# Optimization experiments

Measured on AMD Instinct MI355X. Metric: run time of the kernel, lower is better.

## Reference

```python
import jax, jax.numpy as jnp
import numpy as np

NUM_SPIXELS = 256
N_ITER = 3
TEMP = 1.0


def setup_inputs() -> dict:
    key = jax.random.key(0)
    features = jax.random.normal(key, (4, 16, 256, 256), dtype=jnp.float32)
    return {"features": features}


def reference(features):
    B, C, H, W = features.shape
    dt = features.dtype
    # torch.linspace(0, h-1, h)/h == arange(h)/h
    y = jnp.arange(H, dtype=dt) / H
    x = jnp.arange(W, dtype=dt) / W
    mesh_y, mesh_x = jnp.meshgrid(y, x, indexing='ij')  # each [H, W]
    xy = jnp.stack([mesh_x, mesh_y], axis=0)            # [2, H, W]
    xy_b = jnp.broadcast_to(xy, (B, 2, H, W))

    pixel = jnp.concatenate([features, xy_b], axis=1).reshape(B, C + 2, H * W)
    p = pixel.transpose(0, 2, 1)  # [B, N, D], D = C+2

    s = max(1, int(NUM_SPIXELS ** 0.5))
    # adaptive_avg_pool2d to (s, s); H, W divisible by s -> exact block mean
    def pool(t):
        D = t.shape[1]
        return t.reshape(B, D, s, H // s, s, W // s).mean(axis=(3, 5)).reshape(B, D, s * s)

    centers = jnp.concatenate([pool(features), pool(xy_b)], axis=1)  # [B, D, M]
    c = centers.transpose(0, 2, 1)  # [B, M, D]

    Q = None
    for i in range(N_ITER):
        # Euclidean cdist: ||p||^2 + ||c||^2 - 2 p.c, clipped and sqrt'ed
        d2 = (jnp.sum(p * p, axis=-1)[:, :, None]
              + jnp.sum(c * c, axis=-1)[:, None, :]
              - 2.0 * jnp.einsum('bnd,bmd->bnm', p, c))
        dist = jnp.sqrt(jnp.maximum(d2, 1e-12))  # [B, N, M]
        Q = jax.nn.softmax(-dist * TEMP, axis=-1)
        if i < N_ITER - 1:
            norm = jnp.sum(Q, axis=1)[:, :, None] + 1e-6        # [B, M, 1]
            c = jnp.einsum('bnm,bnd->bmd', Q, p) / norm         # [B, M, D]

    centers_feat = c[:, :, :C].transpose(0, 2, 1)  # [B, C, M]
    return Q, centers_feat
```

## Files before the change

kernel.cpp:

```cpp
#include <hip/hip_runtime.h>
#include <math.h>

#define BB 4
#define CC 16
#define HH 256
#define WW 256
#define NN (HH*WW)
#define MM 256
#define CROW 20
#define PROW 20
#define PIX 32
#define TSUB 4
#define PIXPERBLK (PIX*TSUB)
#define CHUNKS (NN/PIXPERBLK)

typedef float f32x2 __attribute__((ext_vector_type(2)));

__device__ __forceinline__ f32x2 mk2(float a, float b) { f32x2 r; r.x = a; r.y = b; return r; }
__device__ __forceinline__ f32x2 pk_fma(f32x2 a, f32x2 b, f32x2 c) {
    return __builtin_elementwise_fma(a, b, c);
}

__global__ void init_centers(const float* __restrict__ feat, float* __restrict__ cbuf)
{
    const int b    = blockIdx.x >> 8;
    const int m    = blockIdx.x & 255;
    const int lane = threadIdx.x;
    const int sy = m >> 4, sx = m & 15;

    float cvals[16];
#pragma unroll
    for (int d = 0; d < 16; ++d) {
        float v = 0.f;
#pragma unroll
        for (int k = 0; k < 4; ++k) {
            int q  = lane + (k << 6);
            int py = q >> 4, px = q & 15;
            int n  = (sy*16 + py)*WW + sx*16 + px;
            v += feat[((b*CC + d) << 16) + n];
        }
#pragma unroll
        for (int off = 32; off; off >>= 1) v += __shfl_down(v, off);
        cvals[d] = v * (1.f/256.f);
    }
    if (lane == 0) {
        float* row = cbuf + (b*MM + m)*CROW;
        float cn2 = 0.f;
#pragma unroll
        for (int d = 0; d < 16; ++d) { row[d] = cvals[d]; cn2 = fmaf(cvals[d], cvals[d], cn2); }
        float cx = (sx*16 + 7.5f) * (1.f/256.f);
        float cy = (sy*16 + 7.5f) * (1.f/256.f);
        row[16] = cx; row[17] = cy;
        cn2 = fmaf(cx, cx, cn2);
        cn2 = fmaf(cy, cy, cn2);
        row[18] = cn2;
        row[19] = 0.f;
    }
}

__global__ void build_pt(const float* __restrict__ feat, float* __restrict__ ptbuf)
{
    const int b = blockIdx.x >> 8;
    const int n = ((blockIdx.x & 255) << 8) | threadIdx.x;
    float v[16];
#pragma unroll
    for (int d = 0; d < 16; ++d) v[d] = feat[((b*CC + d) << 16) + n];
    float x = (float)(n & 255) * (1.f/256.f);
    float y = (float)(n >> 8) * (1.f/256.f);
    float pn2 = 0.f;
#pragma unroll
    for (int d = 0; d < 16; ++d) pn2 = fmaf(v[d], v[d], pn2);
    pn2 = fmaf(x, x, pn2);
    pn2 = fmaf(y, y, pn2);
    float4* row = reinterpret_cast<float4*>(ptbuf + (size_t)(b*NN + n)*PROW);
    row[0] = make_float4(v[0],  v[1],  v[2],  v[3]);
    row[1] = make_float4(v[4],  v[5],  v[6],  v[7]);
    row[2] = make_float4(v[8],  v[9],  v[10], v[11]);
    row[3] = make_float4(v[12], v[13], v[14], v[15]);
    row[4] = make_float4(x, y, pn2, 1.0f);
}

template<bool FINAL>
__global__ __launch_bounds__(256, 3)
void ssn_iter(const float* __restrict__ ptbuf, const float* __restrict__ cbuf,
              float* __restrict__ wout)
{
    __shared__ __align__(16) float pls[PIXPERBLK*PROW];
    __shared__ float ssum_s[TSUB][4][16];
    __shared__ float w_s[TSUB][PIX];
    __shared__ float xfer[FINAL ? 4 : 128*41];

    const int tid    = threadIdx.x;
    const int b      = blockIdx.x >> 9;
    const int chunk  = blockIdx.x & (CHUNKS-1);
    const int n_base = chunk * PIXPERBLK;
    const int lane   = tid & 63;
    const int wv     = tid >> 6;
    const int mlo    = tid & 127;
    const int pxbase = (tid >> 7) << 4;

    {
        const float4* src = reinterpret_cast<const float4*>(
            ptbuf + (size_t)(b*NN + n_base)*PROW);
#pragma unroll
        for (int k = 0; k < 3; ++k) {
            int f = tid + (k << 8);
            if (f < PIXPERBLK*PROW/4)
                reinterpret_cast<float4*>(pls)[f] = src[f];
        }
    }

    f32x2 cp0[9], cp1[9]; float cn20, cn21;
    {
        const float4* cv = reinterpret_cast<const float4*>(cbuf + (b*MM + mlo)*CROW);
        float4 a0 = cv[0], a1 = cv[1], a2 = cv[2], a3 = cv[3], a4 = cv[4];
        cp0[0]=mk2(a0.x,a0.y); cp0[1]=mk2(a0.z,a0.w);
        cp0[2]=mk2(a1.x,a1.y); cp0[3]=mk2(a1.z,a1.w);
        cp0[4]=mk2(a2.x,a2.y); cp0[5]=mk2(a2.z,a2.w);
        cp0[6]=mk2(a3.x,a3.y); cp0[7]=mk2(a3.z,a3.w);
        cp0[8]=mk2(a4.x,a4.y); cn20=a4.z;
    }
    {
        const float4* cv = reinterpret_cast<const float4*>(cbuf + (b*MM + mlo + 128)*CROW);
        float4 a0 = cv[0], a1 = cv[1], a2 = cv[2], a3 = cv[3], a4 = cv[4];
        cp1[0]=mk2(a0.x,a0.y); cp1[1]=mk2(a0.z,a0.w);
        cp1[2]=mk2(a1.x,a1.y); cp1[3]=mk2(a1.z,a1.w);
        cp1[4]=mk2(a2.x,a2.y); cp1[5]=mk2(a2.z,a2.w);
        cp1[6]=mk2(a3.x,a3.y); cp1[7]=mk2(a3.z,a3.w);
        cp1[8]=mk2(a4.x,a4.y); cn21=a4.z;
    }

    f32x2 acc0[10], acc1[10];
    if (!FINAL) {
#pragma unroll
        for (int k = 0; k < 10; ++k) { acc0[k] = mk2(0.f,0.f); acc1[k] = mk2(0.f,0.f); }
    }

    const int pxo4 = ((lane&1)<<3) | ((lane&2)<<1) | ((lane&4)>>1) | ((lane&8)>>3);

    __syncthreads();

    for (int t = 0; t < TSUB; ++t) {
        float e0[16], e1[16];
#pragma unroll
        for (int k = 0; k < 16; ++k) {
            const float4* pv = reinterpret_cast<const float4*>(
                &pls[(t*PIX + pxbase + k)*PROW]);
            float4 q0 = pv[0], q1 = pv[1], q2 = pv[2], q3 = pv[3], q4 = pv[4];
            f32x2 u0=mk2(q0.x,q0.y), u1=mk2(q0.z,q0.w), u2=mk2(q1.x,q1.y),
                  u3=mk2(q1.z,q1.w), u4=mk2(q2.x,q2.y), u5=mk2(q2.z,q2.w),
                  u6=mk2(q3.x,q3.y), u7=mk2(q3.z,q3.w), u8=mk2(q4.x,q4.y);
            f32x2 d0 = mk2(0.f,0.f), d1 = mk2(0.f,0.f);
            d0 = pk_fma(u0, cp0[0], d0);  d1 = pk_fma(u0, cp1[0], d1);
            d0 = pk_fma(u1, cp0[1], d0);  d1 = pk_fma(u1, cp1[1], d1);
            d0 = pk_fma(u2, cp0[2], d0);  d1 = pk_fma(u2, cp1[2], d1);
            d0 = pk_fma(u3, cp0[3], d0);  d1 = pk_fma(u3, cp1[3], d1);
            d0 = pk_fma(u4, cp0[4], d0);  d1 = pk_fma(u4, cp1[4], d1);
            d0 = pk_fma(u5, cp0[5], d0);  d1 = pk_fma(u5, cp1[5], d1);
            d0 = pk_fma(u6, cp0[6], d0);  d1 = pk_fma(u6, cp1[6], d1);
            d0 = pk_fma(u7, cp0[7], d0);  d1 = pk_fma(u7, cp1[7], d1);
            d0 = pk_fma(u8, cp0[8], d0);  d1 = pk_fma(u8, cp1[8], d1);
            float d20 = fmaf(-2.f, d0.x + d0.y, q4.z + cn20);
            float d21 = fmaf(-2.f, d1.x + d1.y, q4.z + cn21);
            e0[k] = __expf(-__builtin_amdgcn_sqrtf(fmaxf(d20, 1e-12f)));
            e1[k] = __expf(-__builtin_amdgcn_sqrtf(fmaxf(d21, 1e-12f)));
        }

        float s[8];
        {
            const bool hi = (lane & 1);
#pragma unroll
            for (int k = 0; k < 8; ++k) {
                float a  = e0[k]   + e1[k];
                float bq = e0[k+8] + e1[k+8];
                float recv = __shfl_xor(hi ? a : bq, 1);
                s[k] = (hi ? bq : a) + recv;
            }
        }
#define RS_ROUND(MASK, H) { const bool hi = (lane & (MASK)); \
        _Pragma("unroll") \
        for (int k = 0; k < (H); ++k) { \
            float a = s[k], bq = s[k+(H)]; \
            float recv = __shfl_xor(hi ? a : bq, (MASK)); \
            s[k] = (hi ? bq : a) + recv; } }
        RS_ROUND(2, 4)
        RS_ROUND(4, 2)
        RS_ROUND(8, 1)
#undef RS_ROUND
        s[0] += __shfl_xor(s[0], 16);
        s[0] += __shfl_xor(s[0], 32);
        if (lane < 16) ssum_s[t][wv][pxo4] = s[0];
        __syncthreads();
        if (tid < 32) {
            int h = tid >> 4, p4 = tid & 15;
            w_s[t][tid] = 1.0f / (ssum_s[t][2*h][p4] + ssum_s[t][2*h+1][p4]);
        }
        __syncthreads();

        if (FINAL) {
#pragma unroll
            for (int k = 0; k < 16; ++k) {
                float w = w_s[t][pxbase + k];
                size_t rowoff = ((size_t)(b*NN + n_base + t*PIX + pxbase + k) << 8);
                wout[rowoff + mlo]       = e0[k] * w;
                wout[rowoff + mlo + 128] = e1[k] * w;
            }
        } else {
#pragma unroll
            for (int k = 0; k < 16; ++k) {
                const float4* pv = reinterpret_cast<const float4*>(
                    &pls[(t*PIX + pxbase + k)*PROW]);
                float4 q0 = pv[0], q1 = pv[1], q2 = pv[2], q3 = pv[3], q4 = pv[4];
                float w = w_s[t][pxbase + k];
                float w0 = e0[k]*w, w1 = e1[k]*w;
                f32x2 ew0 = mk2(w0, w0), ew1 = mk2(w1, w1);
                f32x2 u0=mk2(q0.x,q0.y), u1=mk2(q0.z,q0.w), u2=mk2(q1.x,q1.y),
                      u3=mk2(q1.z,q1.w), u4=mk2(q2.x,q2.y), u5=mk2(q2.z,q2.w),
                      u6=mk2(q3.x,q3.y), u7=mk2(q3.z,q3.w), u8=mk2(q4.x,q4.y),
                      u9=mk2(q4.z,q4.w);
                acc0[0] = pk_fma(ew0, u0, acc0[0]);  acc1[0] = pk_fma(ew1, u0, acc1[0]);
                acc0[1] = pk_fma(ew0, u1, acc0[1]);  acc1[1] = pk_fma(ew1, u1, acc1[1]);
                acc0[2] = pk_fma(ew0, u2, acc0[2]);  acc1[2] = pk_fma(ew1, u2, acc1[2]);
                acc0[3] = pk_fma(ew0, u3, acc0[3]);  acc1[3] = pk_fma(ew1, u3, acc1[3]);
                acc0[4] = pk_fma(ew0, u4, acc0[4]);  acc1[4] = pk_fma(ew1, u4, acc1[4]);
                acc0[5] = pk_fma(ew0, u5, acc0[5]);  acc1[5] = pk_fma(ew1, u5, acc1[5]);
                acc0[6] = pk_fma(ew0, u6, acc0[6]);  acc1[6] = pk_fma(ew1, u6, acc1[6]);
                acc0[7] = pk_fma(ew0, u7, acc0[7]);  acc1[7] = pk_fma(ew1, u7, acc1[7]);
                acc0[8] = pk_fma(ew0, u8, acc0[8]);  acc1[8] = pk_fma(ew1, u8, acc1[8]);
                acc0[9] = pk_fma(ew0, u9, acc0[9]);  acc1[9] = pk_fma(ew1, u9, acc1[9]);
            }
        }
    }

    if (!FINAL) {
        if (tid >= 128) {
            float* xb = &xfer[(tid - 128)*41];
#pragma unroll
            for (int j = 0; j < 10; ++j) { xb[2*j]    = acc0[j].x; xb[2*j+1]    = acc0[j].y; }
#pragma unroll
            for (int j = 0; j < 10; ++j) { xb[20+2*j] = acc1[j].x; xb[20+2*j+1] = acc1[j].y; }
        }
        __syncthreads();
        if (tid < 128) {
            const float* xb = &xfer[tid*41];
#pragma unroll
            for (int j = 0; j < 10; ++j) { acc0[j].x += xb[2*j];    acc0[j].y += xb[2*j+1]; }
#pragma unroll
            for (int j = 0; j < 10; ++j) { acc1[j].x += xb[20+2*j]; acc1[j].y += xb[20+2*j+1]; }

            float* dst0 = wout + ((size_t)(b*CHUNKS + chunk)*MM + mlo)*PROW;
            float4* v0 = reinterpret_cast<float4*>(dst0);
            v0[0] = make_float4(acc0[0].x, acc0[0].y, acc0[1].x, acc0[1].y);
            v0[1] = make_float4(acc0[2].x, acc0[2].y, acc0[3].x, acc0[3].y);
            v0[2] = make_float4(acc0[4].x, acc0[4].y, acc0[5].x, acc0[5].y);
            v0[3] = make_float4(acc0[6].x, acc0[6].y, acc0[7].x, acc0[7].y);
            v0[4] = make_float4(acc0[8].x, acc0[8].y, acc0[9].y, 0.f);

            float* dst1 = wout + ((size_t)(b*CHUNKS + chunk)*MM + mlo + 128)*PROW;
            float4* v1 = reinterpret_cast<float4*>(dst1);
            v1[0] = make_float4(acc1[0].x, acc1[0].y, acc1[1].x, acc1[1].y);
            v1[1] = make_float4(acc1[2].x, acc1[2].y, acc1[3].x, acc1[3].y);
            v1[2] = make_float4(acc1[4].x, acc1[4].y, acc1[5].x, acc1[5].y);
            v1[3] = make_float4(acc1[6].x, acc1[6].y, acc1[7].x, acc1[7].y);
            v1[4] = make_float4(acc1[8].x, acc1[8].y, acc1[9].y, 0.f);
        }
    }
}

__global__ __launch_bounds__(256)
void reduce_finalize(const float* __restrict__ pp, float* __restrict__ cbuf,
                     float* __restrict__ cfout, int write_cf)
{
    const int b   = blockIdx.x >> 8;
    const int m   = blockIdx.x & 255;
    const int tid = threadIdx.x;
    const int lane = tid & 63, wv = tid >> 6;

    const float4* r0 = reinterpret_cast<const float4*>(
        pp + ((size_t)(b*CHUNKS + tid)*MM + m)*PROW);
    const float4* r1 = reinterpret_cast<const float4*>(
        pp + ((size_t)(b*CHUNKS + tid + 256)*MM + m)*PROW);
    float a[19];
    {
        float4 u0=r0[0], u1=r0[1], u2=r0[2], u3=r0[3], u4=r0[4];
        float4 w0=r1[0], w1=r1[1], w2=r1[2], w3=r1[3], w4=r1[4];
        a[0]=u0.x+w0.x;  a[1]=u0.y+w0.y;  a[2]=u0.z+w0.z;  a[3]=u0.w+w0.w;
        a[4]=u1.x+w1.x;  a[5]=u1.y+w1.y;  a[6]=u1.z+w1.z;  a[7]=u1.w+w1.w;
        a[8]=u2.x+w2.x;  a[9]=u2.y+w2.y;  a[10]=u2.z+w2.z; a[11]=u2.w+w2.w;
        a[12]=u3.x+w3.x; a[13]=u3.y+w3.y; a[14]=u3.z+w3.z; a[15]=u3.w+w3.w;
        a[16]=u4.x+w4.x; a[17]=u4.y+w4.y; a[18]=u4.z+w4.z;
    }
#pragma unroll
    for (int off = 32; off; off >>= 1) {
#pragma unroll
        for (int d = 0; d < 19; ++d) a[d] += __shfl_down(a[d], off);
    }

    __shared__ float red[4][20];
    if (lane == 0) {
#pragma unroll
        for (int d = 0; d < 19; ++d) red[wv][d] = a[d];
    }
    __syncthreads();
    if (tid == 0) {
        float s[19];
#pragma unroll
        for (int d = 0; d < 19; ++d)
            s[d] = red[0][d] + red[1][d] + red[2][d] + red[3][d];
        float den = s[18] + 1e-6f;
        float* row = cbuf + (b*MM + m)*CROW;
        float cn2 = 0.f;
#pragma unroll
        for (int d = 0; d < 18; ++d) {
            float cv = s[d] / den;
            row[d] = cv;
            cn2 = fmaf(cv, cv, cn2);
            if (write_cf && d < 16) cfout[((b*CC + d) << 8) + m] = cv;
        }
        row[18] = cn2;
        row[19] = 0.f;
    }
}

extern "C" void kernel_launch(void* const* d_in, const int* in_sizes, int n_in,
                              void* d_out, int out_size, void* d_ws, size_t ws_size,
                              hipStream_t stream)
{
    const float* feat = (const float*)d_in[0];
    float* dout = (float*)d_out;

    float* cbuf  = (float*)d_ws;
    float* ptbuf = cbuf + 32768;
    float* pp    = ptbuf + (size_t)BB*NN*PROW;

    float* qout  = dout;
    float* cfout = dout + (size_t)BB*NN*MM;

    build_pt<<<dim3(BB*256), dim3(256), 0, stream>>>(feat, ptbuf);
    init_centers<<<dim3(BB*MM), dim3(64), 0, stream>>>(feat, cbuf);

    for (int it = 0; it < 2; ++it) {
        ssn_iter<false><<<dim3(BB*CHUNKS), dim3(256), 0, stream>>>(ptbuf, cbuf, pp);
        reduce_finalize<<<dim3(BB*MM), dim3(256), 0, stream>>>(pp, cbuf, cfout, it == 1);
    }
    ssn_iter<true><<<dim3(BB*CHUNKS), dim3(256), 0, stream>>>(ptbuf, cbuf, qout);
}
```

Measured before the change: 273.7 us.

## Split final SSN pass into dedicated kernel with 4-centers-per-thread mapping

Splits the templated iteration kernel in two: an unchanged non-final kernel and a new final kernel that writes the soft-assignment matrix Q. In the final kernel each thread handles 4 centers strided by 16 and 8 pixels strided by 4, replacing the old 2 centers by 16 contiguous pixels. The shuffle reduction and shared-memory row-sum layout are reworked to match. The aim is to change the Q store pattern and the per-thread work split in the write-bound final pass, at the cost of more center registers per thread and a new reduction mapping.

```diff
diff --git a/kernel.cpp b/kernel.cpp
--- a/kernel.cpp
+++ b/kernel.cpp
@@ -80,15 +80,14 @@
     row[4] = make_float4(x, y, pn2, 1.0f);
 }
 
-template<bool FINAL>
 __global__ __launch_bounds__(256, 3)
-void ssn_iter(const float* __restrict__ ptbuf, const float* __restrict__ cbuf,
-              float* __restrict__ wout)
+void ssn_nf(const float* __restrict__ ptbuf, const float* __restrict__ cbuf,
+            float* __restrict__ pp)
 {
     __shared__ __align__(16) float pls[PIXPERBLK*PROW];
     __shared__ float ssum_s[TSUB][4][16];
     __shared__ float w_s[TSUB][PIX];
-    __shared__ float xfer[FINAL ? 4 : 128*41];
+    __shared__ float xfer[128*41];
 
     const int tid    = threadIdx.x;
     const int b      = blockIdx.x >> 9;
@@ -131,10 +130,8 @@
     }
 
     f32x2 acc0[10], acc1[10];
-    if (!FINAL) {
-#pragma unroll
-        for (int k = 0; k < 10; ++k) { acc0[k] = mk2(0.f,0.f); acc1[k] = mk2(0.f,0.f); }
-    }
+#pragma unroll
+    for (int k = 0; k < 10; ++k) { acc0[k] = mk2(0.f,0.f); acc1[k] = mk2(0.f,0.f); }
 
     const int pxo4 = ((lane&1)<<3) | ((lane&2)<<1) | ((lane&4)>>1) | ((lane&8)>>3);
 
@@ -197,72 +194,180 @@
         }
         __syncthreads();
 
-        if (FINAL) {
-#pragma unroll
-            for (int k = 0; k < 16; ++k) {
-                float w = w_s[t][pxbase + k];
-                size_t rowoff = ((size_t)(b*NN + n_base + t*PIX + pxbase + k) << 8);
-                wout[rowoff + mlo]       = e0[k] * w;
-                wout[rowoff + mlo + 128] = e1[k] * w;
-            }
-        } else {
-#pragma unroll
-            for (int k = 0; k < 16; ++k) {
-                const float4* pv = reinterpret_cast<const float4*>(
-                    &pls[(t*PIX + pxbase + k)*PROW]);
-                float4 q0 = pv[0], q1 = pv[1], q2 = pv[2], q3 = pv[3], q4 = pv[4];
-                float w = w_s[t][pxbase + k];
-                float w0 = e0[k]*w, w1 = e1[k]*w;
-                f32x2 ew0 = mk2(w0, w0), ew1 = mk2(w1, w1);
-                f32x2 u0=mk2(q0.x,q0.y), u1=mk2(q0.z,q0.w), u2=mk2(q1.x,q1.y),
-                      u3=mk2(q1.z,q1.w), u4=mk2(q2.x,q2.y), u5=mk2(q2.z,q2.w),
-                      u6=mk2(q3.x,q3.y), u7=mk2(q3.z,q3.w), u8=mk2(q4.x,q4.y),
-                      u9=mk2(q4.z,q4.w);
-                acc0[0] = pk_fma(ew0, u0, acc0[0]);  acc1[0] = pk_fma(ew1, u0, acc1[0]);
-                acc0[1] = pk_fma(ew0, u1, acc0[1]);  acc1[1] = pk_fma(ew1, u1, acc1[1]);
-                acc0[2] = pk_fma(ew0, u2, acc0[2]);  acc1[2] = pk_fma(ew1, u2, acc1[2]);
-                acc0[3] = pk_fma(ew0, u3, acc0[3]);  acc1[3] = pk_fma(ew1, u3, acc1[3]);
-                acc0[4] = pk_fma(ew0, u4, acc0[4]);  acc1[4] = pk_fma(ew1, u4, acc1[4]);
-                acc0[5] = pk_fma(ew0, u5, acc0[5]);  acc1[5] = pk_fma(ew1, u5, acc1[5]);
-                acc0[6] = pk_fma(ew0, u6, acc0[6]);  acc1[6] = pk_fma(ew1, u6, acc1[6]);
-                acc0[7] = pk_fma(ew0, u7, acc0[7]);  acc1[7] = pk_fma(ew1, u7, acc1[7]);
-                acc0[8] = pk_fma(ew0, u8, acc0[8]);  acc1[8] = pk_fma(ew1, u8, acc1[8]);
-                acc0[9] = pk_fma(ew0, u9, acc0[9]);  acc1[9] = pk_fma(ew1, u9, acc1[9]);
-            }
-        }
-    }
-
-    if (!FINAL) {
-        if (tid >= 128) {
-            float* xb = &xfer[(tid - 128)*41];
-#pragma unroll
-            for (int j = 0; j < 10; ++j) { xb[2*j]    = acc0[j].x; xb[2*j+1]    = acc0[j].y; }
-#pragma unroll
-            for (int j = 0; j < 10; ++j) { xb[20+2*j] = acc1[j].x; xb[20+2*j+1] = acc1[j].y; }
+#pragma unroll
+        for (int k = 0; k < 16; ++k) {
+            const float4* pv = reinterpret_cast<const float4*>(
+                &pls[(t*PIX + pxbase + k)*PROW]);
+            float4 q0 = pv[0], q1 = pv[1], q2 = pv[2], q3 = pv[3], q4 = pv[4];
+            float w = w_s[t][pxbase + k];
+            float w0 = e0[k]*w, w1 = e1[k]*w;
+            f32x2 ew0 = mk2(w0, w0), ew1 = mk2(w1, w1);
+            f32x2 u0=mk2(q0.x,q0.y), u1=mk2(q0.z,q0.w), u2=mk2(q1.x,q1.y),
+                  u3=mk2(q1.z,q1.w), u4=mk2(q2.x,q2.y), u5=mk2(q2.z,q2.w),
+                  u6=mk2(q3.x,q3.y), u7=mk2(q3.z,q3.w), u8=mk2(q4.x,q4.y),
+                  u9=mk2(q4.z,q4.w);
+            acc0[0] = pk_fma(ew0, u0, acc0[0]);  acc1[0] = pk_fma(ew1, u0, acc1[0]);
+            acc0[1] = pk_fma(ew0, u1, acc0[1]);  acc1[1] = pk_fma(ew1, u1, acc1[1]);
+            acc0[2] = pk_fma(ew0, u2, acc0[2]);  acc1[2] = pk_fma(ew1, u2, acc1[2]);
+            acc0[3] = pk_fma(ew0, u3, acc0[3]);  acc1[3] = pk_fma(ew1, u3, acc1[3]);
+            acc0[4] = pk_fma(ew0, u4, acc0[4]);  acc1[4] = pk_fma(ew1, u4, acc1[4]);
+            acc0[5] = pk_fma(ew0, u5, acc0[5]);  acc1[5] = pk_fma(ew1, u5, acc1[5]);
+            acc0[6] = pk_fma(ew0, u6, acc0[6]);  acc1[6] = pk_fma(ew1, u6, acc1[6]);
+            acc0[7] = pk_fma(ew0, u7, acc0[7]);  acc1[7] = pk_fma(ew1, u7, acc1[7]);
+            acc0[8] = pk_fma(ew0, u8, acc0[8]);  acc1[8] = pk_fma(ew1, u8, acc1[8]);
+            acc0[9] = pk_fma(ew0, u9, acc0[9]);  acc1[9] = pk_fma(ew1, u9, acc1[9]);
+        }
+    }
+
+    if (tid >= 128) {
+        float* xb = &xfer[(tid - 128)*41];
+#pragma unroll
+        for (int j = 0; j < 10; ++j) { xb[2*j]    = acc0[j].x; xb[2*j+1]    = acc0[j].y; }
+#pragma unroll
+        for (int j = 0; j < 10; ++j) { xb[20+2*j] = acc1[j].x; xb[20+2*j+1] = acc1[j].y; }
+    }
+    __syncthreads();
+    if (tid < 128) {
+        const float* xb = &xfer[tid*41];
+#pragma unroll
+        for (int j = 0; j < 10; ++j) { acc0[j].x += xb[2*j];    acc0[j].y += xb[2*j+1]; }
+#pragma unroll
+        for (int j = 0; j < 10; ++j) { acc1[j].x += xb[20+2*j]; acc1[j].y += xb[20+2*j+1]; }
+
+        float* dst0 = pp + ((size_t)(b*CHUNKS + chunk)*MM + mlo)*PROW;
+        float4* v0 = reinterpret_cast<float4*>(dst0);
+        v0[0] = make_float4(acc0[0].x, acc0[0].y, acc0[1].x, acc0[1].y);
+        v0[1] = make_float4(acc0[2].x, acc0[2].y, acc0[3].x, acc0[3].y);
+        v0[2] = make_float4(acc0[4].x, acc0[4].y, acc0[5].x, acc0[5].y);
+        v0[3] = make_float4(acc0[6].x, acc0[6].y, acc0[7].x, acc0[7].y);
+        v0[4] = make_float4(acc0[8].x, acc0[8].y, acc0[9].y, 0.f);
+
+        float* dst1 = pp + ((size_t)(b*CHUNKS + chunk)*MM + mlo + 128)*PROW;
+        float4* v1 = reinterpret_cast<float4*>(dst1);
+        v1[0] = make_float4(acc1[0].x, acc1[0].y, acc1[1].x, acc1[1].y);
+        v1[1] = make_float4(acc1[2].x, acc1[2].y, acc1[3].x, acc1[3].y);
+        v1[2] = make_float4(acc1[4].x, acc1[4].y, acc1[5].x, acc1[5].y);
+        v1[3] = make_float4(acc1[6].x, acc1[6].y, acc1[7].x, acc1[7].y);
+        v1[4] = make_float4(acc1[8].x, acc1[8].y, acc1[9].y, 0.f);
+    }
+}
+
+__global__ __launch_bounds__(256, 3)
+void ssn_fin(const float* __restrict__ ptbuf, const float* __restrict__ cbuf,
+             float* __restrict__ qout)
+{
+    __shared__ __align__(16) float pls[PIXPERBLK*PROW];
+    __shared__ float ssum_s[TSUB][4][PIX];
+    __shared__ float w_s[TSUB][PIX];
+
+    const int tid    = threadIdx.x;
+    const int b      = blockIdx.x >> 9;
+    const int chunk  = blockIdx.x & (CHUNKS-1);
+    const int n_base = chunk * PIXPERBLK;
+    const int L      = tid & 63;
+    const int wv     = tid >> 6;
+    const int g      = L & 3;
+    const int msub   = L >> 2;
+    const int mbase  = wv*64 + msub;
+
+    {
+        const float4* src = reinterpret_cast<const float4*>(
+            ptbuf + (size_t)(b*NN + n_base)*PROW);
+#pragma unroll
+        for (int k = 0; k < 3; ++k) {
+            int f = tid + (k << 8);
+            if (f < PIXPERBLK*PROW/4)
+                reinterpret_cast<float4*>(pls)[f] = src[f];
+        }
+    }
+
+    f32x2 cp[4][9]; float cn2[4];
+#pragma unroll
+    for (int j = 0; j < 4; ++j) {
+        const float4* cv = reinterpret_cast<const float4*>(
+            cbuf + (b*MM + mbase + 16*j)*CROW);
+        float4 a0 = cv[0], a1 = cv[1], a2 = cv[2], a3 = cv[3], a4 = cv[4];
+        cp[j][0]=mk2(a0.x,a0.y); cp[j][1]=mk2(a0.z,a0.w);
+        cp[j][2]=mk2(a1.x,a1.y); cp[j][3]=mk2(a1.z,a1.w);
+        cp[j][4]=mk2(a2.x,a2.y); cp[j][5]=mk2(a2.z,a2.w);
+        cp[j][6]=mk2(a3.x,a3.y); cp[j][7]=mk2(a3.z,a3.w);
+        cp[j][8]=mk2(a4.x,a4.y); cn2[j]=a4.z;
+    }
+
+    __syncthreads();
+
+    for (int t = 0; t < TSUB; ++t) {
+        float e[4][8];
+#pragma unroll
+        for (int k = 0; k < 8; ++k) {
+            const int row = t*PIX + g + 4*k;
+            const float4* pv = reinterpret_cast<const float4*>(&pls[row*PROW]);
+            float4 q0 = pv[0], q1 = pv[1], q2 = pv[2], q3 = pv[3], q4 = pv[4];
+            f32x2 u0=mk2(q0.x,q0.y), u1=mk2(q0.z,q0.w), u2=mk2(q1.x,q1.y),
+                  u3=mk2(q1.z,q1.w), u4=mk2(q2.x,q2.y), u5=mk2(q2.z,q2.w),
+                  u6=mk2(q3.x,q3.y), u7=mk2(q3.z,q3.w), u8=mk2(q4.x,q4.y);
+            f32x2 d0=mk2(0.f,0.f), d1=mk2(0.f,0.f), d2v=mk2(0.f,0.f), d3=mk2(0.f,0.f);
+            d0 = pk_fma(u0, cp[0][0], d0); d1 = pk_fma(u0, cp[1][0], d1);
+            d2v= pk_fma(u0, cp[2][0], d2v);d3 = pk_fma(u0, cp[3][0], d3);
+            d0 = pk_fma(u1, cp[0][1], d0); d1 = pk_fma(u1, cp[1][1], d1);
+            d2v= pk_fma(u1, cp[2][1], d2v);d3 = pk_fma(u1, cp[3][1], d3);
+            d0 = pk_fma(u2, cp[0][2], d0); d1 = pk_fma(u2, cp[1][2], d1);
+            d2v= pk_fma(u2, cp[2][2], d2v);d3 = pk_fma(u2, cp[3][2], d3);
+            d0 = pk_fma(u3, cp[0][3], d0); d1 = pk_fma(u3, cp[1][3], d1);
+            d2v= pk_fma(u3, cp[2][3], d2v);d3 = pk_fma(u3, cp[3][3], d3);
+            d0 = pk_fma(u4, cp[0][4], d0); d1 = pk_fma(u4, cp[1][4], d1);
+            d2v= pk_fma(u4, cp[2][4], d2v);d3 = pk_fma(u4, cp[3][4], d3);
+            d0 = pk_fma(u5, cp[0][5], d0); d1 = pk_fma(u5, cp[1][5], d1);
+            d2v= pk_fma(u5, cp[2][5], d2v);d3 = pk_fma(u5, cp[3][5], d3);
+            d0 = pk_fma(u6, cp[0][6], d0); d1 = pk_fma(u6, cp[1][6], d1);
+            d2v= pk_fma(u6, cp[2][6], d2v);d3 = pk_fma(u6, cp[3][6], d3);
+            d0 = pk_fma(u7, cp[0][7], d0); d1 = pk_fma(u7, cp[1][7], d1);
+            d2v= pk_fma(u7, cp[2][7], d2v);d3 = pk_fma(u7, cp[3][7], d3);
+            d0 = pk_fma(u8, cp[0][8], d0); d1 = pk_fma(u8, cp[1][8], d1);
+            d2v= pk_fma(u8, cp[2][8], d2v);d3 = pk_fma(u8, cp[3][8], d3);
+            float s0 = fmaf(-2.f, d0.x + d0.y, q4.z + cn2[0]);
+            float s1 = fmaf(-2.f, d1.x + d1.y, q4.z + cn2[1]);
+            float s2 = fmaf(-2.f, d2v.x + d2v.y, q4.z + cn2[2]);
+            float s3 = fmaf(-2.f, d3.x + d3.y, q4.z + cn2[3]);
+            e[0][k] = __expf(-__builtin_amdgcn_sqrtf(fmaxf(s0, 1e-12f)));
+            e[1][k] = __expf(-__builtin_amdgcn_sqrtf(fmaxf(s1, 1e-12f)));
+            e[2][k] = __expf(-__builtin_amdgcn_sqrtf(fmaxf(s2, 1e-12f)));
+            e[3][k] = __expf(-__builtin_amdgcn_sqrtf(fmaxf(s3, 1e-12f)));
+        }
+
+        float s[8];
+#pragma unroll
+        for (int k = 0; k < 8; ++k)
+            s[k] = (e[0][k] + e[1][k]) + (e[2][k] + e[3][k]);
+#define RS_ROUND(MASK, H) { const bool hi = (L & (MASK)); \
+        _Pragma("unroll") \
+        for (int k = 0; k < (H); ++k) { \
+            float a = s[k], bq = s[k+(H)]; \
+            float recv = __shfl_xor(hi ? a : bq, (MASK)); \
+            s[k] = (hi ? bq : a) + recv; } }
+        RS_ROUND(4, 4)
+        RS_ROUND(8, 2)
+        RS_ROUND(16, 1)
+#undef RS_ROUND
+        s[0] += __shfl_xor(s[0], 32);
+        {
+            const int kown = (((L>>2)&1)<<2) | (((L>>3)&1)<<1) | ((L>>4)&1);
+            if (L < 32) ssum_s[t][wv][g + 4*kown] = s[0];
         }
         __syncthreads();
-        if (tid < 128) {
-            const float* xb = &xfer[tid*41];
-#pragma unroll
-            for (int j = 0; j < 10; ++j) { acc0[j].x += xb[2*j];    acc0[j].y += xb[2*j+1]; }
-#pragma unroll
-            for (int j = 0; j < 10; ++j) { acc1[j].x += xb[20+2*j]; acc1[j].y += xb[20+2*j+1]; }
-
-            float* dst0 = wout + ((size_t)(b*CHUNKS + chunk)*MM + mlo)*PROW;
-            float4* v0 = reinterpret_cast<float4*>(dst0);
-            v0[0] = make_float4(acc0[0].x, acc0[0].y, acc0[1].x, acc0[1].y);
-            v0[1] = make_float4(acc0[2].x, acc0[2].y, acc0[3].x, acc0[3].y);
-            v0[2] = make_float4(acc0[4].x, acc0[4].y, acc0[5].x, acc0[5].y);
-            v0[3] = make_float4(acc0[6].x, acc0[6].y, acc0[7].x, acc0[7].y);
-            v0[4] = make_float4(acc0[8].x, acc0[8].y, acc0[9].y, 0.f);
-
-            float* dst1 = wout + ((size_t)(b*CHUNKS + chunk)*MM + mlo + 128)*PROW;
-            float4* v1 = reinterpret_cast<float4*>(dst1);
-            v1[0] = make_float4(acc1[0].x, acc1[0].y, acc1[1].x, acc1[1].y);
-            v1[1] = make_float4(acc1[2].x, acc1[2].y, acc1[3].x, acc1[3].y);
-            v1[2] = make_float4(acc1[4].x, acc1[4].y, acc1[5].x, acc1[5].y);
-            v1[3] = make_float4(acc1[6].x, acc1[6].y, acc1[7].x, acc1[7].y);
-            v1[4] = make_float4(acc1[8].x, acc1[8].y, acc1[9].y, 0.f);
+        if (tid < 32) {
+            w_s[t][tid] = 1.0f / (ssum_s[t][0][tid] + ssum_s[t][1][tid]
+                                + ssum_s[t][2][tid] + ssum_s[t][3][tid]);
+        }
+        __syncthreads();
+
+#pragma unroll
+        for (int k = 0; k < 8; ++k) {
+            float w = w_s[t][g + 4*k];
+            size_t rowoff = ((size_t)(b*NN + n_base + t*PIX + g + 4*k)) << 8;
+#pragma unroll
+            for (int j = 0; j < 4; ++j)
+                qout[rowoff + mbase + 16*j] = e[j][k] * w;
         }
     }
 }
@@ -340,8 +445,8 @@
     init_centers<<<dim3(BB*MM), dim3(64), 0, stream>>>(feat, cbuf);
 
     for (int it = 0; it < 2; ++it) {
-        ssn_iter<false><<<dim3(BB*CHUNKS), dim3(256), 0, stream>>>(ptbuf, cbuf, pp);
+        ssn_nf<<<dim3(BB*CHUNKS), dim3(256), 0, stream>>>(ptbuf, cbuf, pp);
         reduce_finalize<<<dim3(BB*MM), dim3(256), 0, stream>>>(pp, cbuf, cfout, it == 1);
     }
-    ssn_iter<true><<<dim3(BB*CHUNKS), dim3(256), 0, stream>>>(ptbuf, cbuf, qout);
-}
+    ssn_fin<<<dim3(BB*CHUNKS), dim3(256), 0, stream>>>(ptbuf, cbuf, qout);
+}
```

Result: no change. 275.1 us (+0.5%).

## Compute final-iteration distances with split-bf16 MFMA in a dedicated kernel

Applied to the files above, without the earlier changes.

Splits the templated iteration kernel into a non-final kernel (unchanged logic) and a new final kernel. The final kernel computes pixel-center dot products with 16x16x32 bf16 MFMA, using a hi/lo bf16 split (three MFMAs) to approximate fp32 accuracy. It then does the exp/softmax normalization and writes Q. This moves the dot-product work from packed FMA to matrix cores, at the cost of some precision and per-pixel conversion overhead.

```diff
diff --git a/kernel.cpp b/kernel.cpp
--- a/kernel.cpp
+++ b/kernel.cpp
@@ -15,10 +15,22 @@
 #define CHUNKS (NN/PIXPERBLK)
 
 typedef float f32x2 __attribute__((ext_vector_type(2)));
+typedef float f32x4v __attribute__((ext_vector_type(4)));
+typedef short bf16x8 __attribute__((ext_vector_type(8)));
 
 __device__ __forceinline__ f32x2 mk2(float a, float b) { f32x2 r; r.x = a; r.y = b; return r; }
 __device__ __forceinline__ f32x2 pk_fma(f32x2 a, f32x2 b, f32x2 c) {
     return __builtin_elementwise_fma(a, b, c);
+}
+
+__device__ __forceinline__ unsigned short f2bf(float f) {
+    unsigned u = __builtin_bit_cast(unsigned, f);
+    unsigned r = (u + 0x7FFFu + ((u >> 16) & 1u)) >> 16;
+    return (unsigned short)r;
+}
+__device__ __forceinline__ float bf2f(unsigned short v) {
+    unsigned u = ((unsigned)v) << 16;
+    return __builtin_bit_cast(float, u);
 }
 
 __global__ void init_centers(const float* __restrict__ feat, float* __restrict__ cbuf)
@@ -80,15 +92,14 @@
     row[4] = make_float4(x, y, pn2, 1.0f);
 }
 
-template<bool FINAL>
 __global__ __launch_bounds__(256, 3)
-void ssn_iter(const float* __restrict__ ptbuf, const float* __restrict__ cbuf,
-              float* __restrict__ wout)
+void ssn_nf(const float* __restrict__ ptbuf, const float* __restrict__ cbuf,
+            float* __restrict__ pp)
 {
     __shared__ __align__(16) float pls[PIXPERBLK*PROW];
     __shared__ float ssum_s[TSUB][4][16];
     __shared__ float w_s[TSUB][PIX];
-    __shared__ float xfer[FINAL ? 4 : 128*41];
+    __shared__ float xfer[128*41];
 
     const int tid    = threadIdx.x;
     const int b      = blockIdx.x >> 9;
@@ -131,10 +142,8 @@
     }
 
     f32x2 acc0[10], acc1[10];
-    if (!FINAL) {
-#pragma unroll
-        for (int k = 0; k < 10; ++k) { acc0[k] = mk2(0.f,0.f); acc1[k] = mk2(0.f,0.f); }
-    }
+#pragma unroll
+    for (int k = 0; k < 10; ++k) { acc0[k] = mk2(0.f,0.f); acc1[k] = mk2(0.f,0.f); }
 
     const int pxo4 = ((lane&1)<<3) | ((lane&2)<<1) | ((lane&4)>>1) | ((lane&8)>>3);
 
@@ -197,72 +206,203 @@
         }
         __syncthreads();
 
-        if (FINAL) {
-#pragma unroll
-            for (int k = 0; k < 16; ++k) {
-                float w = w_s[t][pxbase + k];
-                size_t rowoff = ((size_t)(b*NN + n_base + t*PIX + pxbase + k) << 8);
-                wout[rowoff + mlo]       = e0[k] * w;
-                wout[rowoff + mlo + 128] = e1[k] * w;
+#pragma unroll
+        for (int k = 0; k < 16; ++k) {
+            const float4* pv = reinterpret_cast<const float4*>(
+                &pls[(t*PIX + pxbase + k)*PROW]);
+            float4 q0 = pv[0], q1 = pv[1], q2 = pv[2], q3 = pv[3], q4 = pv[4];
+            float w = w_s[t][pxbase + k];
+            float w0 = e0[k]*w, w1 = e1[k]*w;
+            f32x2 ew0 = mk2(w0, w0), ew1 = mk2(w1, w1);
+            f32x2 u0=mk2(q0.x,q0.y), u1=mk2(q0.z,q0.w), u2=mk2(q1.x,q1.y),
+                  u3=mk2(q1.z,q1.w), u4=mk2(q2.x,q2.y), u5=mk2(q2.z,q2.w),
+                  u6=mk2(q3.x,q3.y), u7=mk2(q3.z,q3.w), u8=mk2(q4.x,q4.y),
+                  u9=mk2(q4.z,q4.w);
+            acc0[0] = pk_fma(ew0, u0, acc0[0]);  acc1[0] = pk_fma(ew1, u0, acc1[0]);
+            acc0[1] = pk_fma(ew0, u1, acc0[1]);  acc1[1] = pk_fma(ew1, u1, acc1[1]);
+            acc0[2] = pk_fma(ew0, u2, acc0[2]);  acc1[2] = pk_fma(ew1, u2, acc1[2]);
+            acc0[3] = pk_fma(ew0, u3, acc0[3]);  acc1[3] = pk_fma(ew1, u3, acc1[3]);
+            acc0[4] = pk_fma(ew0, u4, acc0[4]);  acc1[4] = pk_fma(ew1, u4, acc1[4]);
+            acc0[5] = pk_fma(ew0, u5, acc0[5]);  acc1[5] = pk_fma(ew1, u5, acc1[5]);
+            acc0[6] = pk_fma(ew0, u6, acc0[6]);  acc1[6] = pk_fma(ew1, u6, acc1[6]);
+            acc0[7] = pk_fma(ew0, u7, acc0[7]);  acc1[7] = pk_fma(ew1, u7, acc1[7]);
+            acc0[8] = pk_fma(ew0, u8, acc0[8]);  acc1[8] = pk_fma(ew1, u8, acc1[8]);
+            acc0[9] = pk_fma(ew0, u9, acc0[9]);  acc1[9] = pk_fma(ew1, u9, acc1[9]);
+        }
+    }
+
+    if (tid >= 128) {
+        float* xb = &xfer[(tid - 128)*41];
+#pragma unroll
+        for (int j = 0; j < 10; ++j) { xb[2*j]    = acc0[j].x; xb[2*j+1]    = acc0[j].y; }
+#pragma unroll
+        for (int j = 0; j < 10; ++j) { xb[20+2*j] = acc1[j].x; xb[20+2*j+1] = acc1[j].y; }
+    }
+    __syncthreads();
+    if (tid < 128) {
+        const float* xb = &xfer[tid*41];
+#pragma unroll
+        for (int j = 0; j < 10; ++j) { acc0[j].x += xb[2*j];    acc0[j].y += xb[2*j+1]; }
+#pragma unroll
+        for (int j = 0; j < 10; ++j) { acc1[j].x += xb[20+2*j]; acc1[j].y += xb[20+2*j+1]; }
+
+        float* dst0 = pp + ((size_t)(b*CHUNKS + chunk)*MM + mlo)*PROW;
+        float4* v0 = reinterpret_cast<float4*>(dst0);
+        v0[0] = make_float4(acc0[0].x, acc0[0].y, acc0[1].x, acc0[1].y);
+        v0[1] = make_float4(acc0[2].x, acc0[2].y, acc0[3].x, acc0[3].y);
+        v0[2] = make_float4(acc0[4].x, acc0[4].y, acc0[5].x, acc0[5].y);
+        v0[3] = make_float4(acc0[6].x, acc0[6].y, acc0[7].x, acc0[7].y);
+        v0[4] = make_float4(acc0[8].x, acc0[8].y, acc0[9].y, 0.f);
+
+        float* dst1 = pp + ((size_t)(b*CHUNKS + chunk)*MM + mlo + 128)*PROW;
+        float4* v1 = reinterpret_cast<float4*>(dst1);
+        v1[0] = make_float4(acc1[0].x, acc1[0].y, acc1[1].x, acc1[1].y);
+        v1[1] = make_float4(acc1[2].x, acc1[2].y, acc1[3].x, acc1[3].y);
+        v1[2] = make_float4(acc1[4].x, acc1[4].y, acc1[5].x, acc1[5].y);
+        v1[3] = make_float4(acc1[6].x, acc1[6].y, acc1[7].x, acc1[7].y);
+        v1[4] = make_float4(acc1[8].x, acc1[8].y, acc1[9].y, 0.f);
+    }
+}
+
+__global__ __launch_bounds__(256, 3)
+void ssn_fin(const float* __restrict__ ptbuf, const float* __restrict__ cbuf,
+             float* __restrict__ qout)
+{
+    __shared__ __align__(16) float pls[PIXPERBLK*PROW];
+    __shared__ float ssum_s[4][32];
+    __shared__ float w_s[32];
+
+    const int tid    = threadIdx.x;
+    const int b      = blockIdx.x >> 9;
+    const int chunk  = blockIdx.x & (CHUNKS-1);
+    const int n_base = chunk * PIXPERBLK;
+    const int L      = tid & 63;
+    const int wv     = tid >> 6;
+    const int g      = L >> 4;
+    const int al     = L & 15;
+
+    {
+        const float4* src = reinterpret_cast<const float4*>(
+            ptbuf + (size_t)(b*NN + n_base)*PROW);
+#pragma unroll
+        for (int k = 0; k < 3; ++k) {
+            int f = tid + (k << 8);
+            if (f < PIXPERBLK*PROW/4)
+                reinterpret_cast<float4*>(pls)[f] = src[f];
+        }
+    }
+
+    bf16x8 bhi[4], blo[4]; float cn2m[4];
+#pragma unroll
+    for (int mt = 0; mt < 4; ++mt) {
+        const float* crow = cbuf + (size_t)(b*MM + wv*64 + mt*16 + al)*CROW;
+        float bf_[8];
+#pragma unroll
+        for (int j = 0; j < 8; ++j) bf_[j] = 0.f;
+        if (g < 2) {
+            float4 c0 = *reinterpret_cast<const float4*>(crow + 8*g);
+            float4 c1 = *reinterpret_cast<const float4*>(crow + 8*g + 4);
+            bf_[0]=c0.x; bf_[1]=c0.y; bf_[2]=c0.z; bf_[3]=c0.w;
+            bf_[4]=c1.x; bf_[5]=c1.y; bf_[6]=c1.z; bf_[7]=c1.w;
+        } else if (g == 2) {
+            float4 c0 = *reinterpret_cast<const float4*>(crow + 16);
+            bf_[0]=c0.x; bf_[1]=c0.y;
+        }
+#pragma unroll
+        for (int j = 0; j < 8; ++j) {
+            unsigned short h = f2bf(bf_[j]);
+            bhi[mt][j] = (short)h;
+            blo[mt][j] = (short)f2bf(bf_[j] - bf2f(h));
+        }
+        cn2m[mt] = crow[18];
+    }
+
+    __syncthreads();
+
+#pragma unroll
+    for (int pair = 0; pair < 4; ++pair) {
+        float e[2][4][4];
+        float part[2][4];
+
+#pragma unroll
+        for (int h = 0; h < 2; ++h) {
+            const int pxt = pair*32 + h*16;
+
+            float af[8];
+#pragma unroll
+            for (int j = 0; j < 8; ++j) af[j] = 0.f;
+            const int abase = (pxt + al)*PROW;
+            if (g < 2) {
+                float4 x0 = *reinterpret_cast<const float4*>(&pls[abase + 8*g]);
+                float4 x1 = *reinterpret_cast<const float4*>(&pls[abase + 8*g + 4]);
+                af[0]=x0.x; af[1]=x0.y; af[2]=x0.z; af[3]=x0.w;
+                af[4]=x1.x; af[5]=x1.y; af[6]=x1.z; af[7]=x1.w;
+            } else if (g == 2) {
+                float4 x0 = *reinterpret_cast<const float4*>(&pls[abase + 16]);
+                af[0]=x0.x; af[1]=x0.y;
             }
-        } else {
-#pragma unroll
-            for (int k = 0; k < 16; ++k) {
-                const float4* pv = reinterpret_cast<const float4*>(
-                    &pls[(t*PIX + pxbase + k)*PROW]);
-                float4 q0 = pv[0], q1 = pv[1], q2 = pv[2], q3 = pv[3], q4 = pv[4];
-                float w = w_s[t][pxbase + k];
-                float w0 = e0[k]*w, w1 = e1[k]*w;
-                f32x2 ew0 = mk2(w0, w0), ew1 = mk2(w1, w1);
-                f32x2 u0=mk2(q0.x,q0.y), u1=mk2(q0.z,q0.w), u2=mk2(q1.x,q1.y),
-                      u3=mk2(q1.z,q1.w), u4=mk2(q2.x,q2.y), u5=mk2(q2.z,q2.w),
-                      u6=mk2(q3.x,q3.y), u7=mk2(q3.z,q3.w), u8=mk2(q4.x,q4.y),
-                      u9=mk2(q4.z,q4.w);
-                acc0[0] = pk_fma(ew0, u0, acc0[0]);  acc1[0] = pk_fma(ew1, u0, acc1[0]);
-                acc0[1] = pk_fma(ew0, u1, acc0[1]);  acc1[1] = pk_fma(ew1, u1, acc1[1]);
-                acc0[2] = pk_fma(ew0, u2, acc0[2]);  acc1[2] = pk_fma(ew1, u2, acc1[2]);
-                acc0[3] = pk_fma(ew0, u3, acc0[3]);  acc1[3] = pk_fma(ew1, u3, acc1[3]);
-                acc0[4] = pk_fma(ew0, u4, acc0[4]);  acc1[4] = pk_fma(ew1, u4, acc1[4]);
-                acc0[5] = pk_fma(ew0, u5, acc0[5]);  acc1[5] = pk_fma(ew1, u5, acc1[5]);
-                acc0[6] = pk_fma(ew0, u6, acc0[6]);  acc1[6] = pk_fma(ew1, u6, acc1[6]);
-                acc0[7] = pk_fma(ew0, u7, acc0[7]);  acc1[7] = pk_fma(ew1, u7, acc1[7]);
-                acc0[8] = pk_fma(ew0, u8, acc0[8]);  acc1[8] = pk_fma(ew1, u8, acc1[8]);
-                acc0[9] = pk_fma(ew0, u9, acc0[9]);  acc1[9] = pk_fma(ew1, u9, acc1[9]);
+            bf16x8 ahi, alo;
+#pragma unroll
+            for (int j = 0; j < 8; ++j) {
+                unsigned short hb = f2bf(af[j]);
+                ahi[j] = (short)hb;
+                alo[j] = (short)f2bf(af[j] - bf2f(hb));
             }
-        }
-    }
-
-    if (!FINAL) {
-        if (tid >= 128) {
-            float* xb = &xfer[(tid - 128)*41];
-#pragma unroll
-            for (int j = 0; j < 10; ++j) { xb[2*j]    = acc0[j].x; xb[2*j+1]    = acc0[j].y; }
-#pragma unroll
-            for (int j = 0; j < 10; ++j) { xb[20+2*j] = acc1[j].x; xb[20+2*j+1] = acc1[j].y; }
+
+            float pn2v[4];
+#pragma unroll
+            for (int r = 0; r < 4; ++r)
+                pn2v[r] = pls[(pxt + 4*g + r)*PROW + 18];
+
+#pragma unroll
+            for (int mt = 0; mt < 4; ++mt) {
+                f32x4v dt = {0.f, 0.f, 0.f, 0.f};
+                dt = __builtin_amdgcn_mfma_f32_16x16x32_bf16(ahi, bhi[mt], dt, 0, 0, 0);
+                dt = __builtin_amdgcn_mfma_f32_16x16x32_bf16(ahi, blo[mt], dt, 0, 0, 0);
+                dt = __builtin_amdgcn_mfma_f32_16x16x32_bf16(alo, bhi[mt], dt, 0, 0, 0);
+#pragma unroll
+                for (int r = 0; r < 4; ++r) {
+                    float d2 = fmaf(-2.f, dt[r], pn2v[r] + cn2m[mt]);
+                    e[h][mt][r] = __expf(-__builtin_amdgcn_sqrtf(fmaxf(d2, 1e-12f)));
+                }
+            }
+#pragma unroll
+            for (int r = 0; r < 4; ++r)
+                part[h][r] = (e[h][0][r] + e[h][1][r]) + (e[h][2][r] + e[h][3][r]);
+        }
+
+#pragma unroll
+        for (int mask = 1; mask <= 8; mask <<= 1) {
+#pragma unroll
+            for (int h = 0; h < 2; ++h)
+#pragma unroll
+                for (int r = 0; r < 4; ++r)
+                    part[h][r] += __shfl_xor(part[h][r], mask);
+        }
+        if (al == 0) {
+#pragma unroll
+            for (int h = 0; h < 2; ++h)
+#pragma unroll
+                for (int r = 0; r < 4; ++r)
+                    ssum_s[wv][h*16 + 4*g + r] = part[h][r];
         }
         __syncthreads();
-        if (tid < 128) {
-            const float* xb = &xfer[tid*41];
-#pragma unroll
-            for (int j = 0; j < 10; ++j) { acc0[j].x += xb[2*j];    acc0[j].y += xb[2*j+1]; }
-#pragma unroll
-            for (int j = 0; j < 10; ++j) { acc1[j].x += xb[20+2*j]; acc1[j].y += xb[20+2*j+1]; }
-
-            float* dst0 = wout + ((size_t)(b*CHUNKS + chunk)*MM + mlo)*PROW;
-            float4* v0 = reinterpret_cast<float4*>(dst0);
-            v0[0] = make_float4(acc0[0].x, acc0[0].y, acc0[1].x, acc0[1].y);
-            v0[1] = make_float4(acc0[2].x, acc0[2].y, acc0[3].x, acc0[3].y);
-            v0[2] = make_float4(acc0[4].x, acc0[4].y, acc0[5].x, acc0[5].y);
-            v0[3] = make_float4(acc0[6].x, acc0[6].y, acc0[7].x, acc0[7].y);
-            v0[4] = make_float4(acc0[8].x, acc0[8].y, acc0[9].y, 0.f);
-
-            float* dst1 = wout + ((size_t)(b*CHUNKS + chunk)*MM + mlo + 128)*PROW;
-            float4* v1 = reinterpret_cast<float4*>(dst1);
-            v1[0] = make_float4(acc1[0].x, acc1[0].y, acc1[1].x, acc1[1].y);
-            v1[1] = make_float4(acc1[2].x, acc1[2].y, acc1[3].x, acc1[3].y);
-            v1[2] = make_float4(acc1[4].x, acc1[4].y, acc1[5].x, acc1[5].y);
-            v1[3] = make_float4(acc1[6].x, acc1[6].y, acc1[7].x, acc1[7].y);
-            v1[4] = make_float4(acc1[8].x, acc1[8].y, acc1[9].y, 0.f);
+        if (tid < 32)
+            w_s[tid] = 1.0f / (ssum_s[0][tid] + ssum_s[1][tid]
+                             + ssum_s[2][tid] + ssum_s[3][tid]);
+        __syncthreads();
+
+#pragma unroll
+        for (int h = 0; h < 2; ++h) {
+#pragma unroll
+            for (int r = 0; r < 4; ++r) {
+                const float w = w_s[h*16 + 4*g + r];
+                const size_t rowoff =
+                    ((size_t)(b*NN + n_base + pair*32 + h*16 + 4*g + r)) << 8;
+#pragma unroll
+                for (int mt = 0; mt < 4; ++mt)
+                    qout[rowoff + wv*64 + mt*16 + al] = e[h][mt][r] * w;
+            }
         }
     }
 }
@@ -340,8 +480,8 @@
     init_centers<<<dim3(BB*MM), dim3(64), 0, stream>>>(feat, cbuf);
 
     for (int it = 0; it < 2; ++it) {
-        ssn_iter<false><<<dim3(BB*CHUNKS), dim3(256), 0, stream>>>(ptbuf, cbuf, pp);
+        ssn_nf<<<dim3(BB*CHUNKS), dim3(256), 0, stream>>>(ptbuf, cbuf, pp);
         reduce_finalize<<<dim3(BB*MM), dim3(256), 0, stream>>>(pp, cbuf, cfout, it == 1);
     }
-    ssn_iter<true><<<dim3(BB*CHUNKS), dim3(256), 0, stream>>>(ptbuf, cbuf, qout);
-}
+    ssn_fin<<<dim3(BB*CHUNKS), dim3(256), 0, stream>>>(ptbuf, cbuf, qout);
+}
```

Measured after the change: 275.1 us. No clear change (+0.5%).
